# Optimization experiments

Hardware: AMD Instinct MI355X
Metric: run time of the kernel (lower is better)

The kernel has to match this reference:

```python
import jax, jax.numpy as jnp
import numpy as np

B, Q, N, D = 16, 64, 16384, 128


def setup_inputs() -> dict:
    key = jax.random.key(0)
    k1, k2, k3 = jax.random.split(key, 3)
    query_vector = jax.random.normal(k1, (B, Q, D), dtype=jnp.float32)
    m_A = jax.random.normal(k2, (B, N, D), dtype=jnp.float32)
    # valid node counts per batch element, in [N//2, N] so masks are non-degenerate
    node_nums = jax.random.randint(k3, (B,), N // 2, N + 1, dtype=jnp.int32)
    return {"query_vector": query_vector, "m_A": m_A, "node_nums": node_nums}


def reference(query_vector, m_A, node_nums):
    # GraphPF.forward with num_supporting_node = -1 (default path).
    # prob_logits: [B, Q, N]
    prob_logits = jnp.einsum("bqd,bnd->bqn", query_vector, m_A)
    neg = jnp.finfo(prob_logits.dtype).min
    # get_attention_mask: additive mask, 0 for valid nodes, finfo.min for padding
    valid = jnp.arange(m_A.shape[1])[None, :] < node_nums[:, None]  # [B, N]
    attention_mask = jnp.where(valid, 0.0, neg).astype(prob_logits.dtype)[:, None, :]
    masked_logits = prob_logits + attention_mask
    prob_soft = jax.nn.softmax(masked_logits, axis=-1)
    res_vector = jnp.einsum("bqn,bnd->bqd", prob_soft, m_A)
    return (res_vector, prob_soft, prob_logits)
```

## Files before the change

kernel.cpp:

```cpp
#include <hip/hip_runtime.h>
#include <math.h>

#define Bn 16
#define Qn 64
#define Nn 16384
#define Dn 128
#define NT 128
#define NTILES (Nn / NT)
#define NCHUNK 512
#define NCHUNKS (Nn / NCHUNK)

#define RES_ELEMS  (Bn * Qn * Dn)
#define SOFT_OFF   (RES_ELEMS)
#define LOG_OFF    (RES_ELEMS + Bn * Qn * Nn)

#define NEGF (-3.4e38f)

typedef __attribute__((ext_vector_type(8))) short short8;
typedef float f32x4 __attribute__((ext_vector_type(4)));

typedef union { unsigned int u[4]; short8 v; } pk8;

__device__ __forceinline__ unsigned short f2bf(float x) {
    unsigned int u = __float_as_uint(x);
    return (unsigned short)((u + 0x7FFF + ((u >> 16) & 1)) >> 16);
}
__device__ __forceinline__ float bf2f(unsigned short h) {
    return __uint_as_float(((unsigned int)h) << 16);
}

__global__ __launch_bounds__(256) void k_logits(
    const float* __restrict__ qv, const float* __restrict__ A,
    const int* __restrict__ nodeNum,
    float* __restrict__ logits,
    float* __restrict__ pmax, float* __restrict__ psum)
{
    const int b = blockIdx.y, tile = blockIdx.x;
    const int n0 = tile * NT;
    const int tid = threadIdx.x;
    const int lane = tid & 63, wave = tid >> 6;
    const int qd = lane >> 4, cc = lane & 15;

    __shared__ __align__(16) unsigned char smem[55296];
    unsigned short* QHI = (unsigned short*)smem;
    unsigned short* QLO = QHI + 64 * 72;
    unsigned short* AHI = QLO + 64 * 72;
    unsigned short* ALO = AHI + 128 * 72;
    float* CB   = (float*)smem;
    float* REDM = ((float*)smem) + 64 * 132;
    float* REDS = REDM + 64 * 17;

    f32x4 acc[4][2];
#pragma unroll
    for (int mi = 0; mi < 4; mi++)
#pragma unroll
        for (int ni = 0; ni < 2; ni++) acc[mi][ni] = 0.f;

    const float* qb = qv + (size_t)b * Qn * Dn;
    const float* Ab = A  + (size_t)b * Nn * Dn + (size_t)n0 * Dn;

    for (int kk = 0; kk < Dn; kk += 64) {
        __syncthreads();
#pragma unroll
        for (int t = 0; t < 4; t++) {
            int u = tid + t * 256;
            int row = u >> 4, c4 = u & 15;
            float4 v = *(const float4*)(qb + row * Dn + kk + c4 * 4);
            ushort4 hi, lo;
            hi.x = f2bf(v.x); lo.x = f2bf(v.x - bf2f(hi.x));
            hi.y = f2bf(v.y); lo.y = f2bf(v.y - bf2f(hi.y));
            hi.z = f2bf(v.z); lo.z = f2bf(v.z - bf2f(hi.z));
            hi.w = f2bf(v.w); lo.w = f2bf(v.w - bf2f(hi.w));
            *(ushort4*)(QHI + row * 72 + c4 * 4) = hi;
            *(ushort4*)(QLO + row * 72 + c4 * 4) = lo;
        }
#pragma unroll
        for (int t = 0; t < 8; t++) {
            int u = tid + t * 256;
            int row = u >> 4, c4 = u & 15;
            float4 v = *(const float4*)(Ab + row * Dn + kk + c4 * 4);
            ushort4 hi, lo;
            hi.x = f2bf(v.x); lo.x = f2bf(v.x - bf2f(hi.x));
            hi.y = f2bf(v.y); lo.y = f2bf(v.y - bf2f(hi.y));
            hi.z = f2bf(v.z); lo.z = f2bf(v.z - bf2f(hi.z));
            hi.w = f2bf(v.w); lo.w = f2bf(v.w - bf2f(hi.w));
            *(ushort4*)(AHI + row * 72 + c4 * 4) = hi;
            *(ushort4*)(ALO + row * 72 + c4 * 4) = lo;
        }
        __syncthreads();
#pragma unroll
        for (int ks = 0; ks < 64; ks += 32) {
            const int ko = ks + qd * 8;
            short8 qh[4], ql[4], ah[2], al[2];
#pragma unroll
            for (int mi = 0; mi < 4; mi++) {
                int r = mi * 16 + cc;
                qh[mi] = *(const short8*)(QHI + r * 72 + ko);
                ql[mi] = *(const short8*)(QLO + r * 72 + ko);
            }
#pragma unroll
            for (int ni = 0; ni < 2; ni++) {
                int r = (wave * 2 + ni) * 16 + cc;
                ah[ni] = *(const short8*)(AHI + r * 72 + ko);
                al[ni] = *(const short8*)(ALO + r * 72 + ko);
            }
#pragma unroll
            for (int mi = 0; mi < 4; mi++)
#pragma unroll
                for (int ni = 0; ni < 2; ni++) {
                    acc[mi][ni] = __builtin_amdgcn_mfma_f32_16x16x32_bf16(
                        ql[mi], ah[ni], acc[mi][ni], 0, 0, 0);
                    acc[mi][ni] = __builtin_amdgcn_mfma_f32_16x16x32_bf16(
                        qh[mi], al[ni], acc[mi][ni], 0, 0, 0);
                    acc[mi][ni] = __builtin_amdgcn_mfma_f32_16x16x32_bf16(
                        qh[mi], ah[ni], acc[mi][ni], 0, 0, 0);
                }
        }
    }

    __syncthreads();
#pragma unroll
    for (int mi = 0; mi < 4; mi++)
#pragma unroll
        for (int ni = 0; ni < 2; ni++)
#pragma unroll
            for (int r = 0; r < 4; r++) {
                int q = mi * 16 + qd * 4 + r;
                int n = (wave * 2 + ni) * 16 + cc;
                CB[q * 132 + n] = acc[mi][ni][r];
            }
    __syncthreads();

    const int nv = nodeNum[b];
#pragma unroll
    for (int t = 0; t < 8; t++) {
        int u = tid + t * 256;
        int q = u >> 5, ng = u & 31;
        float4 v = *(const float4*)(CB + q * 132 + ng * 4);
        *(float4*)(logits + ((size_t)(b * Qn + q)) * Nn + n0 + ng * 4) = v;
    }
#pragma unroll
    for (int t = 0; t < 4; t++) {
        int u = tid + t * 256;
        int q = u >> 4, c = u & 15;
        const float* base = CB + q * 132 + c * 8;
        float m = NEGF;
#pragma unroll
        for (int j = 0; j < 8; j++)
            if (n0 + c * 8 + j < nv) m = fmaxf(m, base[j]);
        float s = 0.f;
#pragma unroll
        for (int j = 0; j < 8; j++)
            if (n0 + c * 8 + j < nv) s += __expf(base[j] - m);
        REDM[q * 17 + c] = m;
        REDS[q * 17 + c] = s;
    }
    __syncthreads();
    if (tid < Qn) {
        int q = tid;
        float M = NEGF;
#pragma unroll
        for (int t = 0; t < 16; t++) M = fmaxf(M, REDM[q * 17 + t]);
        float S = 0.f;
#pragma unroll
        for (int t = 0; t < 16; t++)
            S += REDS[q * 17 + t] * __expf(REDM[q * 17 + t] - M);
        pmax[((size_t)(b * Qn + q)) * NTILES + tile] = M;
        psum[((size_t)(b * Qn + q)) * NTILES + tile] = S;
    }
}

__global__ __launch_bounds__(64) void k_rows(
    const float* __restrict__ pmax, const float* __restrict__ psum,
    float* __restrict__ Mrow, float* __restrict__ invL)
{
    const int row = blockIdx.x;
    const int t = threadIdx.x;
    const float* pm = pmax + (size_t)row * NTILES;
    const float* ps = psum + (size_t)row * NTILES;
    float m0 = pm[t], m1 = pm[t + 64];
    float s0 = ps[t], s1 = ps[t + 64];
    float m = fmaxf(m0, m1);
#pragma unroll
    for (int o = 32; o >= 1; o >>= 1) m = fmaxf(m, __shfl_xor(m, o, 64));
    float s = s0 * __expf(m0 - m) + s1 * __expf(m1 - m);
#pragma unroll
    for (int o = 32; o >= 1; o >>= 1) s += __shfl_xor(s, o, 64);
    if (t == 0) { Mrow[row] = m; invL[row] = 1.0f / s; }
}

__global__ __launch_bounds__(256) void k_pv(
    const float* __restrict__ A, const int* __restrict__ nodeNum,
    const float* __restrict__ logits,
    const float* __restrict__ Mrow, const float* __restrict__ invL,
    float* __restrict__ soft, float* __restrict__ partial)
{
    const int b = blockIdx.y, chunk = blockIdx.x;
    const int tid = threadIdx.x;
    const int lane = tid & 63, wave = tid >> 6;
    const int qd = lane >> 4, cc = lane & 15;

    __shared__ __align__(16) unsigned short PS[64 * 40];
    __shared__ __align__(16) unsigned int  TMP2[16 * 132];
    __shared__ float MS[64], LS[64];

    if (tid < Qn) {
        MS[tid] = Mrow[b * Qn + tid];
        LS[tid] = invL[b * Qn + tid];
    }

    f32x4 acc[4][2];
#pragma unroll
    for (int mi = 0; mi < 4; mi++)
#pragma unroll
        for (int ni = 0; ni < 2; ni++) acc[mi][ni] = 0.f;

    const int nv = nodeNum[b];
    const float* Abase = A + (size_t)b * Nn * Dn;

    for (int s = 0; s < 16; s++) {
        const int n0 = chunk * NCHUNK + s * 32;
        __syncthreads();

#pragma unroll
        for (int t = 0; t < 2; t++) {
            int u = tid + t * 256;
            int q = u >> 3, ng = u & 7;
            size_t go = ((size_t)(b * Qn + q)) * Nn + n0 + ng * 4;
            float4 l4 = *(const float4*)(logits + go);
            float mq = MS[q], iq = LS[q];
            int nb = n0 + ng * 4;
            float4 p;
            p.x = (nb + 0 < nv) ? __expf(l4.x - mq) * iq : 0.f;
            p.y = (nb + 1 < nv) ? __expf(l4.y - mq) * iq : 0.f;
            p.z = (nb + 2 < nv) ? __expf(l4.z - mq) * iq : 0.f;
            p.w = (nb + 3 < nv) ? __expf(l4.w - mq) * iq : 0.f;
            *(float4*)(soft + go) = p;
            unsigned int d0 = (unsigned)f2bf(p.x) | ((unsigned)f2bf(p.y) << 16);
            unsigned int d1 = (unsigned)f2bf(p.z) | ((unsigned)f2bf(p.w) << 16);
            unsigned int* dst = (unsigned int*)(PS + q * 40 + ng * 4);
            dst[0] = d0; dst[1] = d1;
        }
#pragma unroll
        for (int t = 0; t < 2; t++) {
            int u = tid + t * 256;
            int n2 = u >> 5, db = u & 31;
            const float* r0 = Abase + (size_t)(n0 + n2 * 2) * Dn + db * 4;
            float4 a0 = *(const float4*)r0;
            float4 a1 = *(const float4*)(r0 + Dn);
            uint4 w;
            w.x = (unsigned)f2bf(a0.x) | ((unsigned)f2bf(a1.x) << 16);
            w.y = (unsigned)f2bf(a0.y) | ((unsigned)f2bf(a1.y) << 16);
            w.z = (unsigned)f2bf(a0.z) | ((unsigned)f2bf(a1.z) << 16);
            w.w = (unsigned)f2bf(a0.w) | ((unsigned)f2bf(a1.w) << 16);
            *(uint4*)(TMP2 + n2 * 132 + db * 4) = w;
        }
        __syncthreads();

        short8 pf[4];
#pragma unroll
        for (int mi = 0; mi < 4; mi++)
            pf[mi] = *(const short8*)(PS + (mi * 16 + cc) * 40 + qd * 8);
#pragma unroll
        for (int ni = 0; ni < 2; ni++) {
            int d = (wave * 2 + ni) * 16 + cc;
            pk8 bfr;
#pragma unroll
            for (int j = 0; j < 4; j++)
                bfr.u[j] = TMP2[(qd * 4 + j) * 132 + d];
#pragma unroll
            for (int mi = 0; mi < 4; mi++)
                acc[mi][ni] = __builtin_amdgcn_mfma_f32_16x16x32_bf16(
                    pf[mi], bfr.v, acc[mi][ni], 0, 0, 0);
        }
    }

    float* pout = partial + (size_t)chunk * RES_ELEMS + (size_t)(b * Qn) * Dn;
#pragma unroll
    for (int mi = 0; mi < 4; mi++)
#pragma unroll
        for (int ni = 0; ni < 2; ni++)
#pragma unroll
            for (int r = 0; r < 4; r++) {
                int q = mi * 16 + qd * 4 + r;
                int d = (wave * 2 + ni) * 16 + cc;
                pout[q * Dn + d] = acc[mi][ni][r];
            }
}

__global__ __launch_bounds__(256) void k_red(
    const float* __restrict__ partial, float* __restrict__ res)
{
    int g = blockIdx.x * 256 + threadIdx.x;
    float s = 0.f;
#pragma unroll
    for (int t = 0; t < NCHUNKS; t++)
        s += partial[(size_t)t * RES_ELEMS + g];
    res[g] = s;
}

extern "C" void kernel_launch(void* const* d_in, const int* in_sizes, int n_in,
                              void* d_out, int out_size, void* d_ws, size_t ws_size,
                              hipStream_t stream) {
    const float* qv = (const float*)d_in[0];
    const float* A  = (const float*)d_in[1];
    const int*   nn = (const int*)d_in[2];

    float* out    = (float*)d_out;
    float* res    = out;
    float* soft   = out + SOFT_OFF;
    float* logits = out + LOG_OFF;

    float* ws      = (float*)d_ws;
    float* pmax    = ws;
    float* psum    = pmax + (size_t)Bn * Qn * NTILES;
    float* Mrow    = psum + (size_t)Bn * Qn * NTILES;
    float* invL    = Mrow + Bn * Qn;
    float* partial = invL + Bn * Qn;

    dim3 blk(256);
    k_logits<<<dim3(NTILES, Bn), blk, 0, stream>>>(qv, A, nn, logits, pmax, psum);
    k_rows<<<Bn * Qn, 64, 0, stream>>>(pmax, psum, Mrow, invL);
    k_pv<<<dim3(NCHUNKS, Bn), blk, 0, stream>>>(A, nn, logits, Mrow, invL, soft, partial);
    k_red<<<RES_ELEMS / 256, blk, 0, stream>>>(partial, res);
}
```

Baseline: 295.5 us.

## Register-prefetch global loads, swizzle LDS, halve PV chunk size, add occupancy hints

Both the logits and PV kernels now load the next tile's global data into registers while the current tile is converted and computed, so memory latency overlaps with MFMA work. The logits kernel replaces padded LDS rows with an XOR swizzle, which shrinks shared memory and should raise occupancy. NCHUNK is halved so more PV blocks are launched, and launch_bounds gain min-blocks hints. The costs are higher register pressure that may cause spills, and more partial results for the PV reduction to combine.

```diff
diff --git a/kernel.cpp b/kernel.cpp
--- a/kernel.cpp
+++ b/kernel.cpp
@@ -7,7 +7,7 @@
 #define Dn 128
 #define NT 128
 #define NTILES (Nn / NT)
-#define NCHUNK 512
+#define NCHUNK 256
 #define NCHUNKS (Nn / NCHUNK)
 
 #define RES_ELEMS  (Bn * Qn * Dn)
@@ -29,7 +29,11 @@
     return __uint_as_float(((unsigned int)h) << 16);
 }
 
-__global__ __launch_bounds__(256) void k_logits(
+__device__ __forceinline__ int swz(int row, int col) {
+    return row * 64 + (col ^ ((row & 7) << 3));
+}
+
+__global__ __launch_bounds__(256, 3) void k_logits(
     const float* __restrict__ qv, const float* __restrict__ A,
     const int* __restrict__ nodeNum,
     float* __restrict__ logits,
@@ -41,11 +45,11 @@
     const int lane = tid & 63, wave = tid >> 6;
     const int qd = lane >> 4, cc = lane & 15;
 
-    __shared__ __align__(16) unsigned char smem[55296];
+    __shared__ __align__(16) unsigned char smem[49152];
     unsigned short* QHI = (unsigned short*)smem;
-    unsigned short* QLO = QHI + 64 * 72;
-    unsigned short* AHI = QLO + 64 * 72;
-    unsigned short* ALO = AHI + 128 * 72;
+    unsigned short* QLO = QHI + 64 * 64;
+    unsigned short* AHI = QLO + 64 * 64;
+    unsigned short* ALO = AHI + 128 * 64;
     float* CB   = (float*)smem;
     float* REDM = ((float*)smem) + 64 * 132;
     float* REDS = REDM + 64 * 17;
@@ -59,35 +63,49 @@
     const float* qb = qv + (size_t)b * Qn * Dn;
     const float* Ab = A  + (size_t)b * Nn * Dn + (size_t)n0 * Dn;
 
-    for (int kk = 0; kk < Dn; kk += 64) {
-        __syncthreads();
+    const int r16 = tid >> 4, c4 = tid & 15;
+
+    float4 qreg[4], areg[8];
+
+    auto loadQ = [&](int kk) {
+#pragma unroll
+        for (int t = 0; t < 4; t++)
+            qreg[t] = *(const float4*)(qb + (size_t)(r16 + 16 * t) * Dn + kk + c4 * 4);
+    };
+    auto loadA = [&](int kk) {
+#pragma unroll
+        for (int t = 0; t < 8; t++)
+            areg[t] = *(const float4*)(Ab + (size_t)(r16 + 16 * t) * Dn + kk + c4 * 4);
+    };
+    auto cvtWrite = [&]() {
 #pragma unroll
         for (int t = 0; t < 4; t++) {
-            int u = tid + t * 256;
-            int row = u >> 4, c4 = u & 15;
-            float4 v = *(const float4*)(qb + row * Dn + kk + c4 * 4);
+            int row = r16 + 16 * t;
+            float4 v = qreg[t];
             ushort4 hi, lo;
             hi.x = f2bf(v.x); lo.x = f2bf(v.x - bf2f(hi.x));
             hi.y = f2bf(v.y); lo.y = f2bf(v.y - bf2f(hi.y));
             hi.z = f2bf(v.z); lo.z = f2bf(v.z - bf2f(hi.z));
             hi.w = f2bf(v.w); lo.w = f2bf(v.w - bf2f(hi.w));
-            *(ushort4*)(QHI + row * 72 + c4 * 4) = hi;
-            *(ushort4*)(QLO + row * 72 + c4 * 4) = lo;
+            int idx = swz(row, c4 * 4);
+            *(ushort4*)(QHI + idx) = hi;
+            *(ushort4*)(QLO + idx) = lo;
         }
 #pragma unroll
         for (int t = 0; t < 8; t++) {
-            int u = tid + t * 256;
-            int row = u >> 4, c4 = u & 15;
-            float4 v = *(const float4*)(Ab + row * Dn + kk + c4 * 4);
+            int row = r16 + 16 * t;
+            float4 v = areg[t];
             ushort4 hi, lo;
             hi.x = f2bf(v.x); lo.x = f2bf(v.x - bf2f(hi.x));
             hi.y = f2bf(v.y); lo.y = f2bf(v.y - bf2f(hi.y));
             hi.z = f2bf(v.z); lo.z = f2bf(v.z - bf2f(hi.z));
             hi.w = f2bf(v.w); lo.w = f2bf(v.w - bf2f(hi.w));
-            *(ushort4*)(AHI + row * 72 + c4 * 4) = hi;
-            *(ushort4*)(ALO + row * 72 + c4 * 4) = lo;
-        }
-        __syncthreads();
+            int idx = swz(row, c4 * 4);
+            *(ushort4*)(AHI + idx) = hi;
+            *(ushort4*)(ALO + idx) = lo;
+        }
+    };
+    auto compute = [&]() {
 #pragma unroll
         for (int ks = 0; ks < 64; ks += 32) {
             const int ko = ks + qd * 8;
@@ -95,14 +113,16 @@
 #pragma unroll
             for (int mi = 0; mi < 4; mi++) {
                 int r = mi * 16 + cc;
-                qh[mi] = *(const short8*)(QHI + r * 72 + ko);
-                ql[mi] = *(const short8*)(QLO + r * 72 + ko);
+                int idx = swz(r, ko);
+                qh[mi] = *(const short8*)(QHI + idx);
+                ql[mi] = *(const short8*)(QLO + idx);
             }
 #pragma unroll
             for (int ni = 0; ni < 2; ni++) {
                 int r = (wave * 2 + ni) * 16 + cc;
-                ah[ni] = *(const short8*)(AHI + r * 72 + ko);
-                al[ni] = *(const short8*)(ALO + r * 72 + ko);
+                int idx = swz(r, ko);
+                ah[ni] = *(const short8*)(AHI + idx);
+                al[ni] = *(const short8*)(ALO + idx);
             }
 #pragma unroll
             for (int mi = 0; mi < 4; mi++)
@@ -116,7 +136,17 @@
                         qh[mi], ah[ni], acc[mi][ni], 0, 0, 0);
                 }
         }
-    }
+    };
+
+    loadQ(0); loadA(0);
+    cvtWrite();
+    __syncthreads();
+    loadQ(64); loadA(64);
+    compute();
+    __syncthreads();
+    cvtWrite();
+    __syncthreads();
+    compute();
 
     __syncthreads();
 #pragma unroll
@@ -189,7 +219,7 @@
     if (t == 0) { Mrow[row] = m; invL[row] = 1.0f / s; }
 }
 
-__global__ __launch_bounds__(256) void k_pv(
+__global__ __launch_bounds__(256, 4) void k_pv(
     const float* __restrict__ A, const int* __restrict__ nodeNum,
     const float* __restrict__ logits,
     const float* __restrict__ Mrow, const float* __restrict__ invL,
@@ -218,18 +248,39 @@
     const int nv = nodeNum[b];
     const float* Abase = A + (size_t)b * Nn * Dn;
 
-    for (int s = 0; s < 16; s++) {
+    const int q0 = tid >> 3, ngc = tid & 7;
+    const int n20 = tid >> 5, db = tid & 31;
+
+    float4 l4r[2], a0r[2], a1r[2];
+
+    auto issue = [&](int s) {
+        const int n0 = chunk * NCHUNK + s * 32;
+#pragma unroll
+        for (int t = 0; t < 2; t++) {
+            int q = q0 + 32 * t;
+            l4r[t] = *(const float4*)(logits + ((size_t)(b * Qn + q)) * Nn + n0 + ngc * 4);
+        }
+#pragma unroll
+        for (int t = 0; t < 2; t++) {
+            const float* r0 = Abase + (size_t)(n0 + (n20 + 8 * t) * 2) * Dn + db * 4;
+            a0r[t] = *(const float4*)r0;
+            a1r[t] = *(const float4*)(r0 + Dn);
+        }
+    };
+
+    issue(0);
+
+    for (int s = 0; s < NCHUNK / 32; s++) {
         const int n0 = chunk * NCHUNK + s * 32;
         __syncthreads();
 
 #pragma unroll
         for (int t = 0; t < 2; t++) {
-            int u = tid + t * 256;
-            int q = u >> 3, ng = u & 7;
-            size_t go = ((size_t)(b * Qn + q)) * Nn + n0 + ng * 4;
-            float4 l4 = *(const float4*)(logits + go);
+            int q = q0 + 32 * t;
+            size_t go = ((size_t)(b * Qn + q)) * Nn + n0 + ngc * 4;
+            float4 l4 = l4r[t];
             float mq = MS[q], iq = LS[q];
-            int nb = n0 + ng * 4;
+            int nb = n0 + ngc * 4;
             float4 p;
             p.x = (nb + 0 < nv) ? __expf(l4.x - mq) * iq : 0.f;
             p.y = (nb + 1 < nv) ? __expf(l4.y - mq) * iq : 0.f;
@@ -238,16 +289,13 @@
             *(float4*)(soft + go) = p;
             unsigned int d0 = (unsigned)f2bf(p.x) | ((unsigned)f2bf(p.y) << 16);
             unsigned int d1 = (unsigned)f2bf(p.z) | ((unsigned)f2bf(p.w) << 16);
-            unsigned int* dst = (unsigned int*)(PS + q * 40 + ng * 4);
+            unsigned int* dst = (unsigned int*)(PS + q * 40 + ngc * 4);
             dst[0] = d0; dst[1] = d1;
         }
 #pragma unroll
         for (int t = 0; t < 2; t++) {
-            int u = tid + t * 256;
-            int n2 = u >> 5, db = u & 31;
-            const float* r0 = Abase + (size_t)(n0 + n2 * 2) * Dn + db * 4;
-            float4 a0 = *(const float4*)r0;
-            float4 a1 = *(const float4*)(r0 + Dn);
+            int n2 = n20 + 8 * t;
+            float4 a0 = a0r[t], a1 = a1r[t];
             uint4 w;
             w.x = (unsigned)f2bf(a0.x) | ((unsigned)f2bf(a1.x) << 16);
             w.y = (unsigned)f2bf(a0.y) | ((unsigned)f2bf(a1.y) << 16);
@@ -255,6 +303,7 @@
             w.w = (unsigned)f2bf(a0.w) | ((unsigned)f2bf(a1.w) << 16);
             *(uint4*)(TMP2 + n2 * 132 + db * 4) = w;
         }
+        if (s + 1 < NCHUNK / 32) issue(s + 1);
         __syncthreads();
 
         short8 pf[4];
```

Result: slower. 310.8 us (+5.2%).
